# Kernel optimization log

Measured on AMD Instinct MI355X. Metric: run time of the kernel, lower is better.

## Reference

```python
import jax, jax.numpy as jnp
import numpy as np

N = 8192
D_IN = 128
D_OUT = 128
EPS = 1e-06


def setup_inputs() -> dict:
    key = jax.random.key(0)
    k1, k2, k3, k4 = jax.random.split(key, 4)
    x = jax.random.normal(k1, (N, D_IN), dtype=jnp.float32)
    adj = jax.random.uniform(k2, (N, N), dtype=jnp.float32)
    # nn.Linear(in_features, out_features) params, PyTorch default-ish init scale
    bound = 1.0 / np.sqrt(D_IN)
    W = jax.random.uniform(k3, (D_OUT, D_IN), dtype=jnp.float32, minval=-bound, maxval=bound)
    b = jax.random.uniform(k4, (D_OUT,), dtype=jnp.float32, minval=-bound, maxval=bound)
    return {"x": x, "adj": adj, "W": W, "b": b}


def reference(x, adj, W, b):
    # D^{-1/2} A D^{-1/2}: the diag-matmul chain is mathematically a
    # row/col broadcast scale of adj, so express it that way (same math).
    d_inv_sqrt = 1.0 / jnp.sqrt(adj.sum(axis=1) + EPS)  # [N]
    adj_norm = d_inv_sqrt[:, None] * adj * d_inv_sqrt[None, :]  # [N, N]
    h = adj_norm @ x  # [N, D_IN]
    return h @ W.T + b  # [N, D_OUT]
```

## Files before the change

kernel.cpp:

```cpp
#include <hip/hip_runtime.h>
#include <hip/hip_bf16.h>

#define NN 8192
#define DIN 128
#define DOUT 128

typedef __bf16 bf16;
typedef __bf16 bf16x8 __attribute__((ext_vector_type(8)));
typedef float f32x4 __attribute__((ext_vector_type(4)));

__global__ __launch_bounds__(256) void k1_rowsum(const float* __restrict__ adj,
                                                 float* __restrict__ dinv) {
    int row = blockIdx.x;
    int t   = threadIdx.x;
    const float4* p = reinterpret_cast<const float4*>(adj + (size_t)row * NN);
    float s = 0.f;
    #pragma unroll
    for (int i = 0; i < 8; ++i) {
        float4 v = p[t + i * 256];
        s += (v.x + v.y) + (v.z + v.w);
    }
    #pragma unroll
    for (int off = 32; off > 0; off >>= 1) s += __shfl_down(s, off, 64);
    __shared__ float r4[4];
    if ((t & 63) == 0) r4[t >> 6] = s;
    __syncthreads();
    if (t == 0) dinv[row] = rsqrtf(((r4[0] + r4[1]) + (r4[2] + r4[3])) + 1e-6f);
}

__global__ __launch_bounds__(256) void k2_xwT(const float* __restrict__ x,
                                              const float* __restrict__ W,
                                              const float* __restrict__ dinv,
                                              bf16* __restrict__ yT) {
    __shared__ float Wl[128 * 132];
    __shared__ float xl[32 * 132];
    __shared__ float dl[32];
    int t  = threadIdx.x;
    int i0 = blockIdx.x * 32;
    if (t < 32) dl[t] = dinv[i0 + t];
    #pragma unroll
    for (int s = 0; s < 16; ++s) {
        int i  = t + s * 256;
        int o  = i >> 5;
        int c4 = i & 31;
        *reinterpret_cast<float4*>(&Wl[o * 132 + c4 * 4]) =
            *reinterpret_cast<const float4*>(W + o * 128 + c4 * 4);
    }
    #pragma unroll
    for (int s = 0; s < 4; ++s) {
        int i   = t + s * 256;
        int row = i >> 5;
        int c4  = i & 31;
        *reinterpret_cast<float4*>(&xl[row * 132 + c4 * 4]) =
            *reinterpret_cast<const float4*>(x + (size_t)(i0 + row) * DIN + c4 * 4);
    }
    __syncthreads();
    int o = t & 127;
    int g = t >> 7;
    float acc[16] = {};
    for (int c4 = 0; c4 < 32; ++c4) {
        float4 w4 = *reinterpret_cast<const float4*>(&Wl[o * 132 + c4 * 4]);
        #pragma unroll
        for (int r = 0; r < 16; ++r) {
            float4 h4 = *reinterpret_cast<const float4*>(&xl[(g * 16 + r) * 132 + c4 * 4]);
            acc[r] += h4.x * w4.x + h4.y * w4.y + h4.z * w4.z + h4.w * w4.w;
        }
    }
    bf16x8 o0, o1;
    #pragma unroll
    for (int r = 0; r < 8; ++r) o0[r] = (bf16)(acc[r] * dl[g * 16 + r]);
    #pragma unroll
    for (int r = 0; r < 8; ++r) o1[r] = (bf16)(acc[8 + r] * dl[g * 16 + 8 + r]);
    bf16* dst = yT + (size_t)o * NN + i0 + g * 16;
    *reinterpret_cast<bf16x8*>(dst)     = o0;
    *reinterpret_cast<bf16x8*>(dst + 8) = o1;
}

#define KR3 512
#define LDB3 520

__global__ __launch_bounds__(512, 2) void k3_spmm(const float* __restrict__ adj,
                                                  const bf16* __restrict__ yT,
                                                  const float* __restrict__ dinv,
                                                  float* __restrict__ part) {
    __shared__ bf16 BL[128 * LDB3];
    int t     = threadIdx.x;
    int split = blockIdx.x & 3;
    int mg    = blockIdx.x >> 2;
    int m0    = mg * 128;
    int kbase = split * 2048;

    int wave = t >> 6, lane = t & 63;
    int mrow = lane & 15, quad = lane >> 4;
    int wm0  = m0 + wave * 16;

    f32x4 acc[8] = {};

    for (int cc = 0; cc < 4; ++cc) {
        int kc = kbase + cc * KR3;
        if (cc) __syncthreads();
        for (int i = t; i < 128 * 64; i += 512) {
            int c = i >> 6, ch = i & 63;
            *reinterpret_cast<uint4*>(&BL[c * LDB3 + ch * 8]) =
                *reinterpret_cast<const uint4*>(yT + (size_t)c * NN + kc + ch * 8);
        }
        __syncthreads();

        const float* ap = adj + (size_t)(wm0 + mrow) * NN + kc + quad * 8;
        float4 c0 = *(const float4*)(ap);
        float4 c1 = *(const float4*)(ap + 4);
        float4 n0 = *(const float4*)(ap + 32);
        float4 n1 = *(const float4*)(ap + 36);
        #pragma unroll
        for (int kk = 0; kk < KR3 / 32; ++kk) {
            bf16x8 bf[8];
            int boff = kk * 32 + quad * 8;
            #pragma unroll
            for (int nt = 0; nt < 8; ++nt)
                bf[nt] = *reinterpret_cast<const bf16x8*>(&BL[(nt * 16 + mrow) * LDB3 + boff]);
            int pk = (kk < KR3 / 32 - 2) ? (kk + 2) * 32 : 0;
            float4 f0 = *(const float4*)(ap + pk);
            float4 f1 = *(const float4*)(ap + pk + 4);
            bf16x8 af = { (bf16)c0.x, (bf16)c0.y, (bf16)c0.z, (bf16)c0.w,
                          (bf16)c1.x, (bf16)c1.y, (bf16)c1.z, (bf16)c1.w };
            #pragma unroll
            for (int nt = 0; nt < 8; ++nt)
                acc[nt] = __builtin_amdgcn_mfma_f32_16x16x32_bf16(af, bf[nt], acc[nt], 0, 0, 0);
            c0 = n0; c1 = n1; n0 = f0; n1 = f1;
        }
    }

    f32x4 dv = *reinterpret_cast<const f32x4*>(dinv + wm0 + quad * 4);
    float* pout = part + (size_t)split * (NN * DOUT) + (size_t)wm0 * DOUT;
    #pragma unroll
    for (int nt = 0; nt < 8; ++nt) {
        int col = nt * 16 + mrow;
        #pragma unroll
        for (int r = 0; r < 4; ++r)
            pout[(quad * 4 + r) * DOUT + col] = acc[nt][r] * dv[r];
    }
}

__global__ __launch_bounds__(256) void k4_reduce(const float* __restrict__ part,
                                                 const float* __restrict__ bias,
                                                 float* __restrict__ out) {
    size_t g = (size_t)blockIdx.x * 256 + threadIdx.x;
    float4 s = *reinterpret_cast<const float4*>(bias + (g & 31) * 4);
    #pragma unroll
    for (int sp = 0; sp < 4; ++sp) {
        float4 p = *reinterpret_cast<const float4*>(part + (size_t)sp * NN * DOUT + g * 4);
        s.x += p.x; s.y += p.y; s.z += p.z; s.w += p.w;
    }
    *reinterpret_cast<float4*>(out + g * 4) = s;
}

extern "C" void kernel_launch(void* const* d_in, const int* in_sizes, int n_in,
                              void* d_out, int out_size, void* d_ws, size_t ws_size,
                              hipStream_t stream) {
    const float* x   = (const float*)d_in[0];
    const float* adj = (const float*)d_in[1];
    const float* W   = (const float*)d_in[2];
    const float* b   = (const float*)d_in[3];
    float* out = (float*)d_out;
    char* ws = (char*)d_ws;
    float* dinv = (float*)ws;
    bf16*  yT   = (bf16*)(ws + (1u << 20));
    float* part = (float*)(ws + (4u << 20));

    k1_rowsum<<<NN, 256, 0, stream>>>(adj, dinv);
    k2_xwT   <<<NN / 32, 256, 0, stream>>>(x, W, dinv, yT);
    k3_spmm  <<<4 * (NN / 128), 512, 0, stream>>>(adj, yT, dinv, part);
    k4_reduce<<<(NN * DOUT / 4) / 256, 256, 0, stream>>>(part, b, out);
}
```

Measured before the change: 445.6 us.

## Write bf16 copy of adj during rowsum and stream it in SpMM

The rowsum kernel now also converts adj to bf16 and writes it to workspace, and the SpMM kernel reads that half-size copy instead of the fp32 adj. This takes the conversion out of the MFMA inner loop and halves the bytes the SpMM streams. The cost is an extra 128MB write in the first kernel, so total traffic becomes 256MB read + 128MB write + 128MB read versus 512MB before. Block-to-row mapping in SpMM is also reversed so the most recently written rows are read first, to improve last-level-cache reuse.

```diff
diff --git a/kernel.cpp b/kernel.cpp
--- a/kernel.cpp
+++ b/kernel.cpp
@@ -10,15 +10,22 @@
 typedef float f32x4 __attribute__((ext_vector_type(4)));
 
 __global__ __launch_bounds__(256) void k1_rowsum(const float* __restrict__ adj,
-                                                 float* __restrict__ dinv) {
+                                                 float* __restrict__ dinv,
+                                                 bf16* __restrict__ adjh) {
     int row = blockIdx.x;
     int t   = threadIdx.x;
-    const float4* p = reinterpret_cast<const float4*>(adj + (size_t)row * NN);
+    const float* rp = adj  + (size_t)row * NN;
+    bf16*        hp = adjh + (size_t)row * NN;
     float s = 0.f;
     #pragma unroll
-    for (int i = 0; i < 8; ++i) {
-        float4 v = p[t + i * 256];
-        s += (v.x + v.y) + (v.z + v.w);
+    for (int i = 0; i < 4; ++i) {
+        int base = i * 2048 + t * 8;
+        float4 a = *reinterpret_cast<const float4*>(rp + base);
+        float4 b = *reinterpret_cast<const float4*>(rp + base + 4);
+        s += ((a.x + a.y) + (a.z + a.w)) + ((b.x + b.y) + (b.z + b.w));
+        bf16x8 h = { (bf16)a.x, (bf16)a.y, (bf16)a.z, (bf16)a.w,
+                     (bf16)b.x, (bf16)b.y, (bf16)b.z, (bf16)b.w };
+        *reinterpret_cast<bf16x8*>(hp + base) = h;
     }
     #pragma unroll
     for (int off = 32; off > 0; off >>= 1) s += __shfl_down(s, off, 64);
@@ -79,14 +86,14 @@
 #define KR3 512
 #define LDB3 520
 
-__global__ __launch_bounds__(512, 2) void k3_spmm(const float* __restrict__ adj,
+__global__ __launch_bounds__(512, 2) void k3_spmm(const bf16* __restrict__ adjh,
                                                   const bf16* __restrict__ yT,
                                                   const float* __restrict__ dinv,
                                                   float* __restrict__ part) {
     __shared__ bf16 BL[128 * LDB3];
     int t     = threadIdx.x;
     int split = blockIdx.x & 3;
-    int mg    = blockIdx.x >> 2;
+    int mg    = 63 - (blockIdx.x >> 2);
     int m0    = mg * 128;
     int kbase = split * 2048;
 
@@ -106,11 +113,9 @@
         }
         __syncthreads();
 
-        const float* ap = adj + (size_t)(wm0 + mrow) * NN + kc + quad * 8;
-        float4 c0 = *(const float4*)(ap);
-        float4 c1 = *(const float4*)(ap + 4);
-        float4 n0 = *(const float4*)(ap + 32);
-        float4 n1 = *(const float4*)(ap + 36);
+        const bf16* ap = adjh + (size_t)(wm0 + mrow) * NN + kc + quad * 8;
+        bf16x8 cfr = *reinterpret_cast<const bf16x8*>(ap);
+        bf16x8 nfr = *reinterpret_cast<const bf16x8*>(ap + 32);
         #pragma unroll
         for (int kk = 0; kk < KR3 / 32; ++kk) {
             bf16x8 bf[8];
@@ -119,14 +124,11 @@
             for (int nt = 0; nt < 8; ++nt)
                 bf[nt] = *reinterpret_cast<const bf16x8*>(&BL[(nt * 16 + mrow) * LDB3 + boff]);
             int pk = (kk < KR3 / 32 - 2) ? (kk + 2) * 32 : 0;
-            float4 f0 = *(const float4*)(ap + pk);
-            float4 f1 = *(const float4*)(ap + pk + 4);
-            bf16x8 af = { (bf16)c0.x, (bf16)c0.y, (bf16)c0.z, (bf16)c0.w,
-                          (bf16)c1.x, (bf16)c1.y, (bf16)c1.z, (bf16)c1.w };
+            bf16x8 ffr = *reinterpret_cast<const bf16x8*>(ap + pk);
             #pragma unroll
             for (int nt = 0; nt < 8; ++nt)
-                acc[nt] = __builtin_amdgcn_mfma_f32_16x16x32_bf16(af, bf[nt], acc[nt], 0, 0, 0);
-            c0 = n0; c1 = n1; n0 = f0; n1 = f1;
+                acc[nt] = __builtin_amdgcn_mfma_f32_16x16x32_bf16(cfr, bf[nt], acc[nt], 0, 0, 0);
+            cfr = nfr; nfr = ffr;
         }
     }
 
@@ -166,9 +168,10 @@
     float* dinv = (float*)ws;
     bf16*  yT   = (bf16*)(ws + (1u << 20));
     float* part = (float*)(ws + (4u << 20));
+    bf16*  adjh = (bf16*)(ws + (32u << 20));
 
-    k1_rowsum<<<NN, 256, 0, stream>>>(adj, dinv);
+    k1_rowsum<<<NN, 256, 0, stream>>>(adj, dinv, adjh);
     k2_xwT   <<<NN / 32, 256, 0, stream>>>(x, W, dinv, yT);
-    k3_spmm  <<<4 * (NN / 128), 512, 0, stream>>>(adj, yT, dinv, part);
+    k3_spmm  <<<4 * (NN / 128), 512, 0, stream>>>(adjh, yT, dinv, part);
     k4_reduce<<<(NN * DOUT / 4) / 256, 256, 0, stream>>>(part, b, out);
 }
```

After: 446.6 us. Within noise of the previous version (+0.2%).
